# Kernel tuning notes

Hardware: AMD Instinct MI355X
Metric: run time of the kernel (lower is better)

The kernel has to match this reference:

```python
import jax, jax.numpy as jnp
import numpy as np

D = 128        # hidden dim d
ED = 16        # edge_dim (Time2Vec width)
L = 2          # layers
N_BV, N_LT, N_CM, N_DN = 100000, 20000, 2000, 100000
E0, E1, E2, E3 = 600000, 200000, 500000, 200000
W_SCALE = 0.02


def setup_inputs() -> dict:
    key = jax.random.key(0)
    ks = jax.random.split(key, 24)
    rn = lambda i, s: jax.random.normal(ks[i], s, dtype=jnp.float32)
    ri = lambda i, e, hi: jax.random.randint(ks[i], (e,), 0, hi, dtype=jnp.int32)
    return {
        # node features per type
        "h_bv": rn(0, (N_BV, D)), "h_lt": rn(1, (N_LT, D)),
        "h_cm": rn(2, (N_CM, D)), "h_dn": rn(3, (N_DN, D)),
        # Time2Vec edge features per edge type
        "ft0": rn(4, (E0, ED)), "ft1": rn(5, (E1, ED)),
        "ft2": rn(6, (E2, ED)), "ft3": rn(7, (E3, ED)),
        # per-layer, per-edge-type conv Linear(2d, d)
        "conv_W": rn(8, (L, 4, 2 * D, D)) * W_SCALE,
        "conv_b": jnp.zeros((L, 4, D), jnp.float32),
        # per-edge-type edge MLP Linear(edge_dim, d)
        "emlp_W": rn(9, (4, ED, D)) * W_SCALE,
        "emlp_b": jnp.zeros((4, D), jnp.float32),
        # per-node-type LayerNorm params (order: bv, lt, cm, dn)
        "ln_g": jnp.ones((4, D), jnp.float32),
        "ln_b": jnp.zeros((4, D), jnp.float32),
        # edge indices (src -> dst): voted_on lt->bv, rev_read cm->bv,
        # donated_to dn->lt, read bv->cm
        "src0": ri(10, E0, N_LT), "dst0": ri(11, E0, N_BV),
        "src1": ri(12, E1, N_CM), "dst1": ri(13, E1, N_BV),
        "src2": ri(14, E2, N_DN), "dst2": ri(15, E2, N_LT),
        "src3": ri(16, E3, N_BV), "dst3": ri(17, E3, N_CM),
    }


def _seg_mean(x, idx, n):
    # scatter_mean: segment sum divided by counts (empty segments -> 0)
    s = jax.ops.segment_sum(x, idx, num_segments=n)
    c = jax.ops.segment_sum(jnp.ones((idx.shape[0],), x.dtype), idx, num_segments=n)
    return s / jnp.maximum(c, 1.0)[:, None]


def _layernorm(x, g, b, eps=1e-5):
    m = jnp.mean(x, -1, keepdims=True)
    v = jnp.var(x, -1, keepdims=True)
    return (x - m) * jax.lax.rsqrt(v + eps) * g + b


def reference(h_bv, h_lt, h_cm, h_dn, ft0, ft1, ft2, ft3,
              conv_W, conv_b, emlp_W, emlp_b, ln_g, ln_b,
              src0, dst0, src1, dst1, src2, dst2, src3, dst3):
    # node-type order: 0=bill_version, 1=legislator_term, 2=committee, 3=donor
    h = [h_bv, h_lt, h_cm, h_dn]
    # (et_idx, src_nt, dst_nt, src_idx, dst_idx, edge_time_feat)
    edges = [(0, 1, 0, src0, dst0, ft0),
             (1, 2, 0, src1, dst1, ft1),
             (2, 3, 1, src2, dst2, ft2),
             (3, 0, 2, src3, dst3, ft3)]
    n_layers = conv_W.shape[0]
    for l in range(n_layers):
        out = [jnp.zeros_like(x) for x in h]
        for (e, si, di, src, dst, ft) in edges:
            n_dst = h[di].shape[0]
            agg = _seg_mean(h[si][src], dst, n_dst)          # [N_dst, d]
            cat = jnp.concatenate([h[di], agg], axis=-1)     # [N_dst, 2d]
            y = cat @ conv_W[l, e] + conv_b[l, e]            # [N_dst, d]
            bias = ft @ emlp_W[e] + emlp_b[e]                # [E, d]
            y = y + _seg_mean(bias, dst, n_dst)
            out[di] = out[di] + y
        # drop=0.0 -> dropout is identity
        h = [_layernorm(out[i], ln_g[i], ln_b[i]) for i in range(4)]
    return tuple(h)
```

## Files before the change

kernel.cpp:

```cpp
#include <hip/hip_runtime.h>

typedef short v8s __attribute__((ext_vector_type(8)));
typedef float v4f __attribute__((ext_vector_type(4)));

#define S_I 100352

#define DEG_B   0ull
#define OFF_B   1605632ull
#define CUR_B   3211264ull
#define CSRS_B  4816896ull
#define CSRE_B  10817024ull
#define FTS_B   16817152ull
#define BSUM_B  31025152ull
#define BPRE_B  31033344ull
#define WT_B    31041536ull
#define WEXT_B  31500288ull
#define VROW_B  31598592ull
#define AEXT_B  31599104ull
#define HA_B    47215104ull
#define ZA_B    104047104ull
#define HO_B    160879104ull
#define WS_NEEDED 192111104ull

__device__ __forceinline__ unsigned short f2bf(float f) {
    unsigned u = __float_as_uint(f);
    u += 0x7fffu + ((u >> 16) & 1u);
    return (unsigned short)(u >> 16);
}
__device__ __forceinline__ float bf2f(unsigned short h) {
    return __uint_as_float(((unsigned)h) << 16);
}

struct IPtr4 { const int* p[4]; };
struct IPtr8 { const int* s[4]; const int* d[4]; };
struct FPtr4 { const float* p[4]; };


__global__ void hist_all(IPtr4 dst, int* __restrict__ deg) {
    int i = blockIdx.x * 256 + threadIdx.x;
    if (i >= 1500000) return;
    int e, li;
    if (i < 600000)       { e = 0; li = i; }
    else if (i < 800000)  { e = 1; li = i - 600000; }
    else if (i < 1300000) { e = 2; li = i - 800000; }
    else                  { e = 3; li = i - 1300000; }
    atomicAdd(&deg[e * S_I + dst.p[e][li]], 1);
}

__device__ __forceinline__ void blk_decode(int b, int& e, int& lb, int& N) {
    if (b < 98)       { e = 0; lb = b;       N = 100000; }
    else if (b < 196) { e = 1; lb = b - 98;  N = 100000; }
    else if (b < 216) { e = 2; lb = b - 196; N = 20000;  }
    else              { e = 3; lb = b - 216; N = 2000;   }
}

__global__ void scan_p1(const int* __restrict__ deg, int* __restrict__ bsum) {
    int tid = threadIdx.x;
    int e, lb, N;
    blk_decode(blockIdx.x, e, lb, N);
    const int* dg = deg + e * S_I;
    int base = lb * 1024 + tid * 4;
    int s = 0;
#pragma unroll
    for (int j = 0; j < 4; j++) { int i = base + j; if (i < N) s += dg[i]; }
    for (int o = 32; o > 0; o >>= 1) s += __shfl_down(s, o);
    __shared__ int wsm[4];
    if ((tid & 63) == 0) wsm[tid >> 6] = s;
    __syncthreads();
    if (tid == 0) bsum[e * 512 + lb] = wsm[0] + wsm[1] + wsm[2] + wsm[3];
}

__global__ void scan_p2(const int* __restrict__ bsum, int* __restrict__ bpre, int* __restrict__ off) {
    __shared__ int sh[256];
    int tid = threadIdx.x;
    for (int e = 0; e < 4; e++) {
        int nb = (e < 2) ? 98 : (e == 2 ? 20 : 2);
        int N  = (e < 2) ? 100000 : (e == 2 ? 20000 : 2000);
        int v = (tid < nb) ? bsum[e * 512 + tid] : 0;
        sh[tid] = v;
        __syncthreads();
        for (int s = 1; s < 256; s <<= 1) {
            int t = (tid >= s) ? sh[tid - s] : 0;
            __syncthreads();
            sh[tid] += t;
            __syncthreads();
        }
        if (tid < nb) bpre[e * 512 + tid] = sh[tid] - v;
        if (tid == 0) off[e * S_I + N] = sh[255];
        __syncthreads();
    }
}

__global__ void scan_p3(const int* __restrict__ deg, const int* __restrict__ bpre,
                        int* __restrict__ off, int* __restrict__ cur) {
    int tid = threadIdx.x;
    int e, lb, N;
    blk_decode(blockIdx.x, e, lb, N);
    const int* dg = deg + e * S_I;
    int base = lb * 1024 + tid * 4;
    int v[4], s = 0;
#pragma unroll
    for (int j = 0; j < 4; j++) { int i = base + j; v[j] = (i < N) ? dg[i] : 0; s += v[j]; }
    int lane = tid & 63, w = tid >> 6;
    int sc = s;
    for (int d = 1; d < 64; d <<= 1) { int t = __shfl_up(sc, d); if (lane >= d) sc += t; }
    __shared__ int wsm[4];
    if (lane == 63) wsm[w] = sc;
    __syncthreads();
    int wpre = 0;
    for (int ww = 0; ww < 4; ww++) if (ww < w) wpre += wsm[ww];
    int run = bpre[e * 512 + lb] + wpre + (sc - s);
#pragma unroll
    for (int j = 0; j < 4; j++) {
        int i = base + j;
        if (i < N) { off[e * S_I + i] = run; cur[e * S_I + i] = run; }
        run += v[j];
    }
}

__global__ void fillcsr_all(IPtr8 sd, int* __restrict__ cur,
                            int* __restrict__ csr_src, int* __restrict__ csr_eid) {
    int i = blockIdx.x * 256 + threadIdx.x;
    if (i >= 1500000) return;
    int e, li, eo;
    if (i < 600000)       { e = 0; li = i;           eo = 0; }
    else if (i < 800000)  { e = 1; li = i - 600000;  eo = 600000; }
    else if (i < 1300000) { e = 2; li = i - 800000;  eo = 800000; }
    else                  { e = 3; li = i - 1300000; eo = 1300000; }
    int d = sd.d[e][li];
    int p = atomicAdd(&cur[e * S_I + d], 1);
    csr_src[eo + p] = sd.s[e][li];
    csr_eid[eo + p] = li;
}

__global__ void ftpull_all(FPtr4 ft, const int* __restrict__ csr_eid,
                           const int* __restrict__ off, float* __restrict__ fts) {
    int gid = blockIdx.x * 256 + threadIdx.x;
    int wid = gid >> 6, lane = gid & 63;
    if (wid >= 222000) return;
    int e, n, eo;
    if (wid < 100000)      { e = 0; n = wid;          eo = 0; }
    else if (wid < 200000) { e = 1; n = wid - 100000; eo = 600000; }
    else if (wid < 220000) { e = 2; n = wid - 200000; eo = 800000; }
    else                   { e = 3; n = wid - 220000; eo = 1300000; }
    int s = off[e * S_I + n], t = off[e * S_I + n + 1];
    int sub = lane >> 4, k = lane & 15;
    const float* fp = ft.p[e];
    const int* ep = csr_eid + eo;
    float a0 = 0.f, a1 = 0.f;
    int j = s + sub;
    for (; j + 4 < t; j += 8) {
        int i0 = ep[j], i1 = ep[j + 4];
        a0 += fp[(long long)i0 * 16 + k];
        a1 += fp[(long long)i1 * 16 + k];
    }
    if (j < t) a0 += fp[(long long)ep[j] * 16 + k];
    float a = a0 + a1;
    a += __shfl_down(a, 32);
    a += __shfl_down(a, 16);
    if (lane < 16) fts[(long long)wid * 16 + k] = a;
}

__global__ void wprep(const float* __restrict__ convW, unsigned short* __restrict__ wt) {
    int i = blockIdx.x * 256 + threadIdx.x;
    if (i >= 229376) return;
    int l = i / 114688;
    int rem = i - l * 114688;
    int slot = rem >> 14;
    int idx = rem & 16383;
    int c = idx >> 7, k = idx & 127;
    float v;
    if (slot < 4)
        v = convW[((size_t)(l * 4 + slot) * 256 + 128 + k) * 128 + c];
    else if (slot == 4)
        v = convW[((size_t)(l * 4 + 0) * 256 + k) * 128 + c] +
            convW[((size_t)(l * 4 + 1) * 256 + k) * 128 + c];
    else
        v = convW[((size_t)(l * 4 + (slot - 3)) * 256 + k) * 128 + c];
    wt[i] = f2bf(v);
}

__global__ void wext_build(const float* __restrict__ emlpW, const float* __restrict__ emlpb,
                           const float* __restrict__ convb, unsigned short* __restrict__ wext) {
    int gid = blockIdx.x * 256 + threadIdx.x;
    if (gid >= 49152) return;
    int slot = gid >> 13;
    int rem = gid & 8191;
    int c = rem >> 6, r = rem & 63;
    int l = slot / 3, t = slot - l * 3;
    int ef = (t == 0) ? 0 : (t == 1) ? 2 : 3;
    int rr = r & 31, half = r >> 5;
    int e = (t == 0) ? (half ? 1 : 0) : (half ? -1 : ef);
    float v = 0.f;
    if (e >= 0) {
        if (rr < 16)       v = emlpW[e * 2048 + rr * 128 + c];
        else if (rr == 16) v = emlpb[e * 128 + c];
    }
    if (r == 62) {
        v = convb[(l * 4 + ef) * 128 + c];
        if (t == 0) v += convb[(l * 4 + 1) * 128 + c];
    }
    wext[(long long)slot * 8192 + c * 64 + r] = f2bf(v);
}

__global__ void aext_build(const int* __restrict__ off, const float* __restrict__ fts,
                           unsigned short* __restrict__ aext) {
    int gid = blockIdx.x * 256 + threadIdx.x;
    if (gid >= 7808000) return;
    int wid = gid >> 6, c = gid & 63;
    int t, n;
    if (wid < 100000)      { t = 0; n = wid; }
    else if (wid < 120000) { t = 1; n = wid - 100000; }
    else                   { t = 2; n = wid - 120000; }
    int cc = c & 31, half = c >> 5;
    int e = -1;
    if (t == 0) e = half ? 1 : 0;
    else if (half == 0) e = (t == 1) ? 2 : 3;
    float v = 0.f;
    if (e >= 0) {
        int s = off[e * S_I + n], en = off[e * S_I + n + 1];
        int dg = en - s;
        if (dg > 0) {
            int fb = (e == 0) ? 0 : (e == 1) ? 100000 : (e == 2) ? 200000 : 220000;
            if (cc < 16)       v = fts[(long long)(fb + n) * 16 + cc] / (float)dg;
            else if (cc == 16) v = 1.f;
        }
    }
    if (c == 62) v = 1.f;
    aext[(long long)wid * 64 + c] = f2bf(v);
}

__global__ void h0cvt(FPtr4 h, unsigned short* __restrict__ ha) {
    long long i4 = ((long long)blockIdx.x * 256 + threadIdx.x) * 4;
    if (i4 >= 28416000ll) return;
    long long r = i4 >> 7;
    int c = (int)(i4 & 127);
    int t; long long lr;
    if (r < 100000)      { t = 0; lr = r; }
    else if (r < 120000) { t = 1; lr = r - 100000; }
    else if (r < 122000) { t = 2; lr = r - 120000; }
    else                 { t = 3; lr = r - 122000; }
    const float4 v = *(const float4*)&h.p[t][lr * 128 + c];
    ushort4 o;
    o.x = f2bf(v.x); o.y = f2bf(v.y); o.z = f2bf(v.z); o.w = f2bf(v.w);
    *(ushort4*)&ha[i4] = o;
}

__global__ void vrow_build(const float* __restrict__ lnb, const unsigned short* __restrict__ wt,
                           float* __restrict__ vrow) {
    int c = threadIdx.x;
    const unsigned short* w = wt + (size_t)(1 * 7 + 2) * 16384 + (size_t)c * 128;
    float s = 0.f;
    for (int k = 0; k < 128; k++) s += bf2f(f2bf(lnb[384 + k])) * bf2f(w[k]);
    vrow[c] = s;
}

__device__ __forceinline__ void acc8(float* t, uint4 v) {
    t[0] += __uint_as_float(v.x << 16);
    t[1] += __uint_as_float(v.x & 0xffff0000u);
    t[2] += __uint_as_float(v.y << 16);
    t[3] += __uint_as_float(v.y & 0xffff0000u);
    t[4] += __uint_as_float(v.z << 16);
    t[5] += __uint_as_float(v.z & 0xffff0000u);
    t[6] += __uint_as_float(v.w << 16);
    t[7] += __uint_as_float(v.w & 0xffff0000u);
}

__global__ __launch_bounds__(256) void pull_all(int l, const int* __restrict__ off,
        const int* __restrict__ csr_src, const unsigned short* __restrict__ za,
        const float* __restrict__ vrow, unsigned short* __restrict__ hout) {
    long long gid = (long long)blockIdx.x * 256 + threadIdx.x;
    int wid = (int)(gid >> 6), lane = (int)(gid & 63);
    if (wid >= 122000) return;
    int t, n;
    if (wid < 100000)      { t = 0; n = wid; }
    else if (wid < 120000) { t = 1; n = wid - 100000; }
    else                   { t = 2; n = wid - 120000; }
    int sub = lane >> 4, k8 = (lane & 15) * 8;
    float a[8];
#pragma unroll
    for (int i = 0; i < 8; i++) a[i] = 0.f;
    int ef = (t == 0) ? 0 : (t == 1) ? 2 : 3;
    int ne = (t == 0) ? 2 : 1;
    for (int ii = 0; ii < ne; ii++) {
        int e = ef + ii;
        int s = off[e * S_I + n], en = off[e * S_I + n + 1];
        int cnt = en - s;
        if (cnt <= 0) continue;
        if (e == 2 && l == 1) {
            if (sub == 0) {
                float4 v0 = *(const float4*)&vrow[k8];
                float4 v1 = *(const float4*)&vrow[k8 + 4];
                a[0] += v0.x; a[1] += v0.y; a[2] += v0.z; a[3] += v0.w;
                a[4] += v1.x; a[5] += v1.y; a[6] += v1.z; a[7] += v1.w;
            }
            continue;
        }
        int eo   = (e == 0) ? 0 : (e == 1) ? 600000 : (e == 2) ? 800000 : 1300000;
        long long zo = (e == 0) ? 0 : (e == 1) ? 20000 : (e == 2) ? 22000 : 122000;
        const int* cs = csr_src + eo + s;
        const unsigned short* zb = za + zo * 128;
        float t0[8], t1[8];
#pragma unroll
        for (int i = 0; i < 8; i++) { t0[i] = 0.f; t1[i] = 0.f; }
        int j = sub;
        for (; j + 4 < cnt; j += 8) {
            int i0 = cs[j], i1 = cs[j + 4];
            uint4 v0 = *(const uint4*)&zb[(long long)i0 * 128 + k8];
            uint4 v1 = *(const uint4*)&zb[(long long)i1 * 128 + k8];
            acc8(t0, v0);
            acc8(t1, v1);
        }
        if (j < cnt) {
            int i0 = cs[j];
            uint4 v0 = *(const uint4*)&zb[(long long)i0 * 128 + k8];
            acc8(t0, v0);
        }
        float inv = 1.f / (float)cnt;
#pragma unroll
        for (int i = 0; i < 8; i++) a[i] += (t0[i] + t1[i]) * inv;
    }
#pragma unroll
    for (int i = 0; i < 8; i++) {
        a[i] += __shfl_xor(a[i], 16);
        a[i] += __shfl_xor(a[i], 32);
    }
    if (sub == 0) {
        uint4 p;
        p.x = (unsigned)f2bf(a[0]) | ((unsigned)f2bf(a[1]) << 16);
        p.y = (unsigned)f2bf(a[2]) | ((unsigned)f2bf(a[3]) << 16);
        p.z = (unsigned)f2bf(a[4]) | ((unsigned)f2bf(a[5]) << 16);
        p.w = (unsigned)f2bf(a[6]) | ((unsigned)f2bf(a[7]) << 16);
        *(uint4*)&hout[(long long)wid * 128 + k8] = p;
    }
}

__global__ __launch_bounds__(256, 2) void zgemm(int l, const unsigned short* __restrict__ ha,
        const unsigned short* __restrict__ wt, unsigned short* __restrict__ za) {
    __shared__ unsigned short As[16384];
    __shared__ unsigned short Bs[16384];
    int b = blockIdx.x;
    int e, lb, M; long long aoff, zoff;
    if (l == 0) {
        if (b < 157)      { e = 0; lb = b;       M = 20000;  aoff = 100000; zoff = 0; }
        else if (b < 173) { e = 1; lb = b - 157; M = 2000;   aoff = 120000; zoff = 20000; }
        else if (b < 955) { e = 2; lb = b - 173; M = 100000; aoff = 122000; zoff = 22000; }
        else              { e = 3; lb = b - 955; M = 100000; aoff = 0;      zoff = 122000; }
    } else {
        if (b < 157)      { e = 0; lb = b;       M = 20000;  aoff = 100000; zoff = 0; }
        else if (b < 173) { e = 1; lb = b - 157; M = 2000;   aoff = 120000; zoff = 20000; }
        else              { e = 3; lb = b - 173; M = 100000; aoff = 0;      zoff = 122000; }
    }
    const unsigned short* A  = ha + aoff * 128;
    const unsigned short* Wt = wt + (size_t)(l * 7 + e) * 16384;
    unsigned short* outb = za + zoff * 128;
    int tid = threadIdx.x;
    long long row0 = (long long)lb * 128;
#pragma unroll
    for (int i = 0; i < 8; i++) {
        int idx = tid + i * 256;
        int m = idx >> 4, c = idx & 15;
        int sw = c ^ (m & 15);
        uint4 va = make_uint4(0u, 0u, 0u, 0u);
        long long gr = row0 + m;
        if (gr < M) va = *(const uint4*)&A[gr * 128 + c * 8];
        *(uint4*)&As[m * 128 + sw * 8] = va;
        uint4 wv = *(const uint4*)&Wt[m * 128 + c * 8];
        *(uint4*)&Bs[m * 128 + sw * 8] = wv;
    }
    __syncthreads();
    int lane = tid & 63, w = tid >> 6;
    int q = lane >> 4, ml = lane & 15;
    v4f acc[2][8];
#pragma unroll
    for (int i = 0; i < 2; i++)
#pragma unroll
        for (int j = 0; j < 8; j++) acc[i][j] = (v4f){0.f, 0.f, 0.f, 0.f};
#pragma unroll
    for (int kc = 0; kc < 4; kc++) {
        int ch = (4 * kc + q) ^ ml;
        v8s af[2], bf[8];
#pragma unroll
        for (int i = 0; i < 2; i++) af[i] = *(const v8s*)&As[(32 * w + 16 * i + ml) * 128 + ch * 8];
#pragma unroll
        for (int j = 0; j < 8; j++) bf[j] = *(const v8s*)&Bs[(16 * j + ml) * 128 + ch * 8];
#pragma unroll
        for (int i = 0; i < 2; i++)
#pragma unroll
            for (int j = 0; j < 8; j++)
                acc[i][j] = __builtin_amdgcn_mfma_f32_16x16x32_bf16(af[i], bf[j], acc[i][j], 0, 0, 0);
    }
#pragma unroll
    for (int i = 0; i < 2; i++)
#pragma unroll
        for (int r = 0; r < 4; r++) {
            long long row = row0 + 32 * w + 16 * i + q * 4 + r;
            if (row < M) {
#pragma unroll
                for (int j = 0; j < 8; j++)
                    outb[row * 128 + 16 * j + ml] = f2bf(acc[i][j][r]);
            }
        }
}

__global__ __launch_bounds__(256, 2) void selfgemm(int l, unsigned short* __restrict__ ha,
        const unsigned short* __restrict__ wt, const unsigned short* __restrict__ wext,
        const unsigned short* __restrict__ aext, const unsigned short* __restrict__ ho,
        float* __restrict__ outf, const float* __restrict__ lng, const float* __restrict__ lnb) {
    __shared__ unsigned short As[16384];
    __shared__ unsigned short Bs[16384];
    int b = blockIdx.x;
    int t, lb, M; long long hoff;
    if (b < 782)      { t = 0; lb = b;       M = 100000; hoff = 0; }
    else if (b < 939) { t = 1; lb = b - 782; M = 20000;  hoff = 100000; }
    else              { t = 2; lb = b - 939; M = 2000;   hoff = 120000; }
    const unsigned short* A    = ha + hoff * 128;
    const unsigned short* Ax   = aext + hoff * 64;
    const unsigned short* Wt_  = wt + (size_t)(l * 7 + 4 + t) * 16384;
    const unsigned short* Wx   = wext + (size_t)(l * 3 + t) * 8192;
    const unsigned short* Cadd = ho + hoff * 128;
    const float* g  = lng + t * 128;
    const float* bb = lnb + t * 128;
    int tid = threadIdx.x;
    long long row0 = (long long)lb * 128;
#pragma unroll
    for (int i = 0; i < 8; i++) {
        int idx = tid + i * 256;
        int m = idx >> 4, c = idx & 15;
        int sw = c ^ (m & 15);
        uint4 va = make_uint4(0u, 0u, 0u, 0u);
        long long gr = row0 + m;
        if (gr < M) va = *(const uint4*)&A[gr * 128 + c * 8];
        *(uint4*)&As[m * 128 + sw * 8] = va;
        uint4 wv = *(const uint4*)&Wt_[m * 128 + c * 8];
        *(uint4*)&Bs[m * 128 + sw * 8] = wv;
    }
    __syncthreads();
    int lane = tid & 63, w = tid >> 6;
    int q = lane >> 4, ml = lane & 15;
    v4f acc[2][8];
#pragma unroll
    for (int i = 0; i < 2; i++)
#pragma unroll
        for (int j = 0; j < 8; j++) acc[i][j] = (v4f){0.f, 0.f, 0.f, 0.f};
#pragma unroll
    for (int kc = 0; kc < 4; kc++) {
        int ch = (4 * kc + q) ^ ml;
        v8s af[2], bf[8];
#pragma unroll
        for (int i = 0; i < 2; i++) af[i] = *(const v8s*)&As[(32 * w + 16 * i + ml) * 128 + ch * 8];
#pragma unroll
        for (int j = 0; j < 8; j++) bf[j] = *(const v8s*)&Bs[(16 * j + ml) * 128 + ch * 8];
#pragma unroll
        for (int i = 0; i < 2; i++)
#pragma unroll
            for (int j = 0; j < 8; j++)
                acc[i][j] = __builtin_amdgcn_mfma_f32_16x16x32_bf16(af[i], bf[j], acc[i][j], 0, 0, 0);
    }
    __syncthreads();
#pragma unroll
    for (int i = 0; i < 4; i++) {
        int idx = tid + i * 256;
        int m = idx >> 3, c = idx & 7;
        int sw = c ^ (m & 7);
        uint4 va = make_uint4(0u, 0u, 0u, 0u);
        long long gr = row0 + m;
        if (gr < M) va = *(const uint4*)&Ax[gr * 64 + c * 8];
        *(uint4*)&As[m * 64 + sw * 8] = va;
        uint4 wv = *(const uint4*)&Wx[m * 64 + c * 8];
        *(uint4*)&Bs[m * 64 + sw * 8] = wv;
    }
    __syncthreads();
#pragma unroll
    for (int kc = 0; kc < 2; kc++) {
        int ch = (4 * kc + q) ^ (ml & 7);
        v8s af[2], bf[8];
#pragma unroll
        for (int i = 0; i < 2; i++) af[i] = *(const v8s*)&As[(32 * w + 16 * i + ml) * 64 + ch * 8];
#pragma unroll
        for (int j = 0; j < 8; j++) bf[j] = *(const v8s*)&Bs[(16 * j + ml) * 64 + ch * 8];
#pragma unroll
        for (int i = 0; i < 2; i++)
#pragma unroll
            for (int j = 0; j < 8; j++)
                acc[i][j] = __builtin_amdgcn_mfma_f32_16x16x32_bf16(af[i], bf[j], acc[i][j], 0, 0, 0);
    }
    float gv[8], bv[8];
#pragma unroll
    for (int j = 0; j < 8; j++) { gv[j] = g[16 * j + ml]; bv[j] = bb[16 * j + ml]; }
    unsigned short* outb = ha + hoff * 128;
    float* outF = outf + hoff * 128;
#pragma unroll
    for (int i = 0; i < 2; i++) {
#pragma unroll
        for (int r = 0; r < 4; r++) {
            long long row = row0 + 32 * w + 16 * i + q * 4 + r;
            bool valid = row < M;
            float s = 0.f, s2 = 0.f;
#pragma unroll
            for (int j = 0; j < 8; j++) {
                float v = acc[i][j][r];
                if (valid) v += bf2f(Cadd[row * 128 + 16 * j + ml]);
                acc[i][j][r] = v;
                s += v; s2 += v * v;
            }
#pragma unroll
            for (int msk = 1; msk < 16; msk <<= 1) {
                s  += __shfl_xor(s,  msk);
                s2 += __shfl_xor(s2, msk);
            }
            float mean = s * 0.0078125f;
            float var  = s2 * 0.0078125f - mean * mean;
            float rs = rsqrtf(var + 1e-5f);
            if (valid) {
#pragma unroll
                for (int j = 0; j < 8; j++) {
                    float v = (acc[i][j][r] - mean) * rs * gv[j] + bv[j];
                    if (l == 0) outb[row * 128 + 16 * j + ml] = f2bf(v);
                    else        outF[row * 128 + 16 * j + ml] = v;
                }
            }
        }
    }
}

__global__ void fill_dn(float* __restrict__ of, const float* __restrict__ lnb3) {
    long long i4 = ((long long)blockIdx.x * 256 + threadIdx.x) * 4;
    if (i4 >= 12800000ll) return;
    int c = (int)(i4 & 127);
    *(float4*)&of[i4] = make_float4(lnb3[c], lnb3[c + 1], lnb3[c + 2], lnb3[c + 3]);
}

extern "C" void kernel_launch(void* const* d_in, const int* in_sizes, int n_in,
                              void* d_out, int out_size, void* d_ws, size_t ws_size,
                              hipStream_t stream) {
    if (ws_size < WS_NEEDED) return;

    const float* h0[4] = {(const float*)d_in[0], (const float*)d_in[1],
                          (const float*)d_in[2], (const float*)d_in[3]};
    const float* ftp[4] = {(const float*)d_in[4], (const float*)d_in[5],
                           (const float*)d_in[6], (const float*)d_in[7]};
    const float* convW = (const float*)d_in[8];
    const float* convb = (const float*)d_in[9];
    const float* emlpW = (const float*)d_in[10];
    const float* emlpb = (const float*)d_in[11];
    const float* lng   = (const float*)d_in[12];
    const float* lnb   = (const float*)d_in[13];
    const int* srcp[4] = {(const int*)d_in[14], (const int*)d_in[16],
                          (const int*)d_in[18], (const int*)d_in[20]};
    const int* dstp[4] = {(const int*)d_in[15], (const int*)d_in[17],
                          (const int*)d_in[19], (const int*)d_in[21]};
    char* ws = (char*)d_ws;
    float* out = (float*)d_out;

    int* deg = (int*)(ws + DEG_B);
    int* off = (int*)(ws + OFF_B);
    int* cur = (int*)(ws + CUR_B);
    int* csr_src = (int*)(ws + CSRS_B);
    int* csr_eid = (int*)(ws + CSRE_B);
    float* fts = (float*)(ws + FTS_B);
    int* bsum = (int*)(ws + BSUM_B);
    int* bpre = (int*)(ws + BPRE_B);
    unsigned short* wt   = (unsigned short*)(ws + WT_B);
    unsigned short* wext = (unsigned short*)(ws + WEXT_B);
    float* vrow = (float*)(ws + VROW_B);
    unsigned short* aext = (unsigned short*)(ws + AEXT_B);
    unsigned short* ha = (unsigned short*)(ws + HA_B);
    unsigned short* za = (unsigned short*)(ws + ZA_B);
    unsigned short* ho = (unsigned short*)(ws + HO_B);

    hipMemsetAsync(deg, 0, 4 * S_I * sizeof(int), stream);
    IPtr4 dsts; for (int e = 0; e < 4; e++) dsts.p[e] = dstp[e];
    hist_all<<<5860, 256, 0, stream>>>(dsts, deg);
    scan_p1<<<218, 256, 0, stream>>>(deg, bsum);
    scan_p2<<<1, 256, 0, stream>>>(bsum, bpre, off);
    scan_p3<<<218, 256, 0, stream>>>(deg, bpre, off, cur);
    IPtr8 sd;
    for (int e = 0; e < 4; e++) { sd.s[e] = srcp[e]; sd.d[e] = dstp[e]; }
    fillcsr_all<<<5860, 256, 0, stream>>>(sd, cur, csr_src, csr_eid);
    FPtr4 ftq; for (int e = 0; e < 4; e++) ftq.p[e] = ftp[e];
    ftpull_all<<<55500, 256, 0, stream>>>(ftq, csr_eid, off, fts);
    wprep<<<896, 256, 0, stream>>>(convW, wt);
    wext_build<<<192, 256, 0, stream>>>(emlpW, emlpb, convb, wext);
    vrow_build<<<1, 128, 0, stream>>>(lnb, wt, vrow);
    FPtr4 hq; for (int t = 0; t < 4; t++) hq.p[t] = h0[t];
    h0cvt<<<27750, 256, 0, stream>>>(hq, ha);
    aext_build<<<30500, 256, 0, stream>>>(off, fts, aext);

    for (int l = 0; l < 2; l++) {
        zgemm<<<(l == 0) ? 1737 : 955, 256, 0, stream>>>(l, ha, wt, za);
        pull_all<<<30500, 256, 0, stream>>>(l, off, csr_src, za, vrow, ho);
        selfgemm<<<955, 256, 0, stream>>>(l, ha, wt, wext, aext, ho, out, lng, lnb);
    }
    fill_dn<<<12500, 256, 0, stream>>>(out + 122000ll * 128, lnb + 384);
}
```

Baseline: 904.6 us.

## Fuse edge-feature segment sum into histogram via atomics; merge constant-prep kernels

Per-destination sums of the Time2Vec edge features are now accumulated with float atomics inside the degree-histogram kernel. This removes the csr_eid array, its writes in fillcsr, and the separate CSR-based ftpull gather kernel. The three small weight-preparation kernels (wprep, wext_build, vrow_build) are merged into one launch, and vrow now reads convW directly instead of the converted bf16 weights. The cost is 24M float atomics into fts plus an extra memset, and float-atomic summation makes the order of accumulation nondeterministic.

```diff
diff --git a/kernel.cpp b/kernel.cpp
--- a/kernel.cpp
+++ b/kernel.cpp
@@ -9,7 +9,6 @@
 #define OFF_B   1605632ull
 #define CUR_B   3211264ull
 #define CSRS_B  4816896ull
-#define CSRE_B  10817024ull
 #define FTS_B   16817152ull
 #define BSUM_B  31025152ull
 #define BPRE_B  31033344ull
@@ -35,16 +34,20 @@
 struct IPtr8 { const int* s[4]; const int* d[4]; };
 struct FPtr4 { const float* p[4]; };
 
-
-__global__ void hist_all(IPtr4 dst, int* __restrict__ deg) {
-    int i = blockIdx.x * 256 + threadIdx.x;
-    if (i >= 1500000) return;
-    int e, li;
-    if (i < 600000)       { e = 0; li = i; }
-    else if (i < 800000)  { e = 1; li = i - 600000; }
-    else if (i < 1300000) { e = 2; li = i - 800000; }
-    else                  { e = 3; li = i - 1300000; }
-    atomicAdd(&deg[e * S_I + dst.p[e][li]], 1);
+__global__ void hist_ft(IPtr4 dst, FPtr4 ft, int* __restrict__ deg, float* __restrict__ fts) {
+    long long gid = (long long)blockIdx.x * 256 + threadIdx.x;
+    if (gid >= 24000000ll) return;
+    int k = (int)(gid & 15);
+    int i = (int)(gid >> 4);
+    int e, li, fb;
+    if (i < 600000)       { e = 0; li = i;           fb = 0; }
+    else if (i < 800000)  { e = 1; li = i - 600000;  fb = 100000; }
+    else if (i < 1300000) { e = 2; li = i - 800000;  fb = 200000; }
+    else                  { e = 3; li = i - 1300000; fb = 220000; }
+    int d = dst.p[e][li];
+    float v = ft.p[e][(long long)li * 16 + k];
+    atomicAdd(&fts[(long long)(fb + d) * 16 + k], v);
+    if (k == 0) atomicAdd(&deg[e * S_I + d], 1);
 }
 
 __device__ __forceinline__ void blk_decode(int b, int& e, int& lb, int& N) {
@@ -118,8 +121,7 @@
     }
 }
 
-__global__ void fillcsr_all(IPtr8 sd, int* __restrict__ cur,
-                            int* __restrict__ csr_src, int* __restrict__ csr_eid) {
+__global__ void fillcsr_all(IPtr8 sd, int* __restrict__ cur, int* __restrict__ csr_src) {
     int i = blockIdx.x * 256 + threadIdx.x;
     if (i >= 1500000) return;
     int e, li, eo;
@@ -130,77 +132,55 @@
     int d = sd.d[e][li];
     int p = atomicAdd(&cur[e * S_I + d], 1);
     csr_src[eo + p] = sd.s[e][li];
-    csr_eid[eo + p] = li;
-}
-
-__global__ void ftpull_all(FPtr4 ft, const int* __restrict__ csr_eid,
-                           const int* __restrict__ off, float* __restrict__ fts) {
+}
+
+__global__ void const_build(const float* __restrict__ convW, const float* __restrict__ emlpW,
+                            const float* __restrict__ emlpb, const float* __restrict__ convb,
+                            const float* __restrict__ lnb, unsigned short* __restrict__ wt,
+                            unsigned short* __restrict__ wext, float* __restrict__ vrow) {
     int gid = blockIdx.x * 256 + threadIdx.x;
-    int wid = gid >> 6, lane = gid & 63;
-    if (wid >= 222000) return;
-    int e, n, eo;
-    if (wid < 100000)      { e = 0; n = wid;          eo = 0; }
-    else if (wid < 200000) { e = 1; n = wid - 100000; eo = 600000; }
-    else if (wid < 220000) { e = 2; n = wid - 200000; eo = 800000; }
-    else                   { e = 3; n = wid - 220000; eo = 1300000; }
-    int s = off[e * S_I + n], t = off[e * S_I + n + 1];
-    int sub = lane >> 4, k = lane & 15;
-    const float* fp = ft.p[e];
-    const int* ep = csr_eid + eo;
-    float a0 = 0.f, a1 = 0.f;
-    int j = s + sub;
-    for (; j + 4 < t; j += 8) {
-        int i0 = ep[j], i1 = ep[j + 4];
-        a0 += fp[(long long)i0 * 16 + k];
-        a1 += fp[(long long)i1 * 16 + k];
-    }
-    if (j < t) a0 += fp[(long long)ep[j] * 16 + k];
-    float a = a0 + a1;
-    a += __shfl_down(a, 32);
-    a += __shfl_down(a, 16);
-    if (lane < 16) fts[(long long)wid * 16 + k] = a;
-}
-
-__global__ void wprep(const float* __restrict__ convW, unsigned short* __restrict__ wt) {
-    int i = blockIdx.x * 256 + threadIdx.x;
-    if (i >= 229376) return;
-    int l = i / 114688;
-    int rem = i - l * 114688;
-    int slot = rem >> 14;
-    int idx = rem & 16383;
-    int c = idx >> 7, k = idx & 127;
-    float v;
-    if (slot < 4)
-        v = convW[((size_t)(l * 4 + slot) * 256 + 128 + k) * 128 + c];
-    else if (slot == 4)
-        v = convW[((size_t)(l * 4 + 0) * 256 + k) * 128 + c] +
-            convW[((size_t)(l * 4 + 1) * 256 + k) * 128 + c];
-    else
-        v = convW[((size_t)(l * 4 + (slot - 3)) * 256 + k) * 128 + c];
-    wt[i] = f2bf(v);
-}
-
-__global__ void wext_build(const float* __restrict__ emlpW, const float* __restrict__ emlpb,
-                           const float* __restrict__ convb, unsigned short* __restrict__ wext) {
-    int gid = blockIdx.x * 256 + threadIdx.x;
-    if (gid >= 49152) return;
-    int slot = gid >> 13;
-    int rem = gid & 8191;
-    int c = rem >> 6, r = rem & 63;
-    int l = slot / 3, t = slot - l * 3;
-    int ef = (t == 0) ? 0 : (t == 1) ? 2 : 3;
-    int rr = r & 31, half = r >> 5;
-    int e = (t == 0) ? (half ? 1 : 0) : (half ? -1 : ef);
-    float v = 0.f;
-    if (e >= 0) {
-        if (rr < 16)       v = emlpW[e * 2048 + rr * 128 + c];
-        else if (rr == 16) v = emlpb[e * 128 + c];
-    }
-    if (r == 62) {
-        v = convb[(l * 4 + ef) * 128 + c];
-        if (t == 0) v += convb[(l * 4 + 1) * 128 + c];
-    }
-    wext[(long long)slot * 8192 + c * 64 + r] = f2bf(v);
+    if (gid < 229376) {
+        int i = gid;
+        int l = i / 114688;
+        int rem = i - l * 114688;
+        int slot = rem >> 14;
+        int idx = rem & 16383;
+        int c = idx >> 7, k = idx & 127;
+        float v;
+        if (slot < 4)
+            v = convW[((size_t)(l * 4 + slot) * 256 + 128 + k) * 128 + c];
+        else if (slot == 4)
+            v = convW[((size_t)(l * 4 + 0) * 256 + k) * 128 + c] +
+                convW[((size_t)(l * 4 + 1) * 256 + k) * 128 + c];
+        else
+            v = convW[((size_t)(l * 4 + (slot - 3)) * 256 + k) * 128 + c];
+        wt[i] = f2bf(v);
+    } else if (gid < 229376 + 49152) {
+        int g = gid - 229376;
+        int slot = g >> 13;
+        int rem = g & 8191;
+        int c = rem >> 6, r = rem & 63;
+        int l = slot / 3, t = slot - l * 3;
+        int ef = (t == 0) ? 0 : (t == 1) ? 2 : 3;
+        int rr = r & 31, half = r >> 5;
+        int e = (t == 0) ? (half ? 1 : 0) : (half ? -1 : ef);
+        float v = 0.f;
+        if (e >= 0) {
+            if (rr < 16)       v = emlpW[e * 2048 + rr * 128 + c];
+            else if (rr == 16) v = emlpb[e * 128 + c];
+        }
+        if (r == 62) {
+            v = convb[(l * 4 + ef) * 128 + c];
+            if (t == 0) v += convb[(l * 4 + 1) * 128 + c];
+        }
+        wext[(long long)slot * 8192 + c * 64 + r] = f2bf(v);
+    } else if (gid < 229376 + 49152 + 128) {
+        int c = gid - 229376 - 49152;
+        float s = 0.f;
+        for (int k = 0; k < 128; k++)
+            s += bf2f(f2bf(lnb[384 + k])) * bf2f(f2bf(convW[((size_t)(1 * 4 + 2) * 256 + 128 + k) * 128 + c]));
+        vrow[c] = s;
+    }
 }
 
 __global__ void aext_build(const int* __restrict__ off, const float* __restrict__ fts,
@@ -246,15 +226,6 @@
     *(ushort4*)&ha[i4] = o;
 }
 
-__global__ void vrow_build(const float* __restrict__ lnb, const unsigned short* __restrict__ wt,
-                           float* __restrict__ vrow) {
-    int c = threadIdx.x;
-    const unsigned short* w = wt + (size_t)(1 * 7 + 2) * 16384 + (size_t)c * 128;
-    float s = 0.f;
-    for (int k = 0; k < 128; k++) s += bf2f(f2bf(lnb[384 + k])) * bf2f(w[k]);
-    vrow[c] = s;
-}
-
 __device__ __forceinline__ void acc8(float* t, uint4 v) {
     t[0] += __uint_as_float(v.x << 16);
     t[1] += __uint_as_float(v.x & 0xffff0000u);
@@ -557,7 +528,6 @@
     int* off = (int*)(ws + OFF_B);
     int* cur = (int*)(ws + CUR_B);
     int* csr_src = (int*)(ws + CSRS_B);
-    int* csr_eid = (int*)(ws + CSRE_B);
     float* fts = (float*)(ws + FTS_B);
     int* bsum = (int*)(ws + BSUM_B);
     int* bpre = (int*)(ws + BPRE_B);
@@ -570,19 +540,20 @@
     unsigned short* ho = (unsigned short*)(ws + HO_B);
 
     hipMemsetAsync(deg, 0, 4 * S_I * sizeof(int), stream);
+    hipMemsetAsync(fts, 0, 222000ull * 16 * sizeof(float), stream);
+
     IPtr4 dsts; for (int e = 0; e < 4; e++) dsts.p[e] = dstp[e];
-    hist_all<<<5860, 256, 0, stream>>>(dsts, deg);
+    FPtr4 ftq;  for (int e = 0; e < 4; e++) ftq.p[e] = ftp[e];
+    hist_ft<<<93750, 256, 0, stream>>>(dsts, ftq, deg, fts);
+
     scan_p1<<<218, 256, 0, stream>>>(deg, bsum);
     scan_p2<<<1, 256, 0, stream>>>(bsum, bpre, off);
     scan_p3<<<218, 256, 0, stream>>>(deg, bpre, off, cur);
     IPtr8 sd;
     for (int e = 0; e < 4; e++) { sd.s[e] = srcp[e]; sd.d[e] = dstp[e]; }
-    fillcsr_all<<<5860, 256, 0, stream>>>(sd, cur, csr_src, csr_eid);
-    FPtr4 ftq; for (int e = 0; e < 4; e++) ftq.p[e] = ftp[e];
-    ftpull_all<<<55500, 256, 0, stream>>>(ftq, csr_eid, off, fts);
-    wprep<<<896, 256, 0, stream>>>(convW, wt);
-    wext_build<<<192, 256, 0, stream>>>(emlpW, emlpb, convb, wext);
-    vrow_build<<<1, 128, 0, stream>>>(lnb, wt, vrow);
+    fillcsr_all<<<5860, 256, 0, stream>>>(sd, cur, csr_src);
+
+    const_build<<<1089, 256, 0, stream>>>(convW, emlpW, emlpb, convb, lnb, wt, wext, vrow);
     FPtr4 hq; for (int t = 0; t < 4; t++) hq.p[t] = h0[t];
     h0cvt<<<27750, 256, 0, stream>>>(hq, ha);
     aext_build<<<30500, 256, 0, stream>>>(off, fts, aext);
```

New measurement: 885.6 us. 1.02x faster.
